# Kernel tuning notes

Hardware: AMD Instinct MI355X
Metric: run time of the kernel (lower is better)

The kernel has to match this reference:

```python
import jax, jax.numpy as jnp
import numpy as np

K = 2  # number of propagation hops (SGConv K)
NEG_SLOPE = 0.1


def setup_inputs() -> dict:
    key = jax.random.key(0)
    k1, k2, k3, k4 = jax.random.split(key, 4)
    N, E, C_in, C_out = 50000, 800000, 128, 512
    x = jax.random.normal(k1, (N, C_in), dtype=jnp.float32)
    edge_index = jax.random.randint(k2, (2, E), 0, N, dtype=jnp.int64)
    W = jax.random.normal(k3, (C_out, C_in), dtype=jnp.float32) * (1.0 / np.sqrt(C_in))
    b = jax.random.normal(k4, (C_out,), dtype=jnp.float32) * 0.01
    return {"x": x, "edge_index": edge_index, "W": W, "b": b}


def reference(x, edge_index, W, b):
    N = x.shape[0]
    # gcn_norm with self-loops (PyG SGConv default: add_self_loops=True)
    loop = jnp.arange(N, dtype=edge_index.dtype)
    src = jnp.concatenate([edge_index[0], loop])  # message sources j
    dst = jnp.concatenate([edge_index[1], loop])  # aggregation targets i
    deg = jax.ops.segment_sum(jnp.ones_like(dst, dtype=x.dtype), dst, num_segments=N)
    dinv = jnp.where(deg > 0, jax.lax.rsqrt(deg), 0.0)
    norm = dinv[src] * dinv[dst]  # [E+N]
    h = x
    for _ in range(K):
        h = jax.ops.segment_sum(norm[:, None] * h[src], dst, num_segments=N)
    y = h @ W.T + b
    return jnp.where(y >= 0, y, NEG_SLOPE * y)  # LeakyReLU(0.1)
```

## Files before the change

kernel.cpp:

```cpp
#include <hip/hip_runtime.h>
#include <hip/hip_bf16.h>

#define CIN 128
#define COUT 512
#define NEG_SLOPE 0.1f

typedef __bf16 bf16x8 __attribute__((ext_vector_type(8)));
typedef float f32x4 __attribute__((ext_vector_type(4)));

static __device__ __forceinline__ unsigned short f2bf(float f) {
  unsigned int u = __builtin_bit_cast(unsigned int, f);
  unsigned int lsb = (u >> 16) & 1u;
  u += 0x7fffu + lsb;
  return (unsigned short)(u >> 16);
}
static __device__ __forceinline__ float bf_lo(unsigned int u) {
  return __builtin_bit_cast(float, u << 16);
}
static __device__ __forceinline__ float bf_hi(unsigned int u) {
  return __builtin_bit_cast(float, u & 0xffff0000u);
}
static __device__ __forceinline__ unsigned int pack2(float lo, float hi) {
  return (unsigned int)f2bf(lo) | ((unsigned int)f2bf(hi) << 16);
}

__global__ void detect_kernel(const int* __restrict__ raw, int* __restrict__ flag, int E) {
  __shared__ int any_nonzero;
  int tid = threadIdx.x;
  if (tid == 0) any_nonzero = 0;
  __syncthreads();
  int v1 = raw[2 * tid + 1];
  int v2 = raw[2 * (E / 2) + 2 * tid + 1];
  if (v1 != 0 || v2 != 0) atomicOr(&any_nonzero, 1);
  __syncthreads();
  if (tid == 0) *flag = any_nonzero ? 0 : 1;
}

__global__ void decode_count_kernel(const int* __restrict__ raw, const int* __restrict__ flag,
                                    int* __restrict__ srcA, int* __restrict__ dstA,
                                    int* __restrict__ cnt, int E, int N) {
  int e = blockIdx.x * blockDim.x + threadIdx.x;
  if (e >= E) return;
  int is64 = *flag;
  int s, d;
  if (is64) {
    s = raw[2 * e];
    d = raw[2 * (E + e)];
  } else {
    s = raw[e];
    d = raw[E + e];
  }
  if ((unsigned)s >= (unsigned)N) s = 0;
  if ((unsigned)d >= (unsigned)N) d = 0;
  srcA[e] = s;
  dstA[e] = d;
  atomicAdd(&cnt[d], 1);
}

__global__ void dinv_kernel(const int* __restrict__ cnt, float* __restrict__ dinv, int N) {
  int i = blockIdx.x * blockDim.x + threadIdx.x;
  if (i < N) dinv[i] = 1.0f / sqrtf((float)(cnt[i] + 1));
}

__global__ __launch_bounds__(256) void xscale_kernel(const float* __restrict__ x,
                                                     const float* __restrict__ dinv,
                                                     unsigned short* __restrict__ xs, int N) {
  int idx = blockIdx.x * blockDim.x + threadIdx.x;
  if (idx >= N * (CIN / 4)) return;
  int row = idx >> 5;
  float d = dinv[row];
  float4 v = ((const float4*)x)[idx];
  ushort4 o;
  o.x = f2bf(v.x * d); o.y = f2bf(v.y * d); o.z = f2bf(v.z * d); o.w = f2bf(v.w * d);
  ((ushort4*)xs)[idx] = o;
}

__global__ __launch_bounds__(256) void scan1_kernel(const int* __restrict__ cnt,
                                                    int* __restrict__ rowptr,
                                                    int* __restrict__ bsum, int N) {
  __shared__ int buf[256];
  int tid = threadIdx.x;
  int base = blockIdx.x * 1024 + tid * 4;
  int v[4];
  int tot = 0;
#pragma unroll
  for (int k = 0; k < 4; ++k) {
    int i = base + k;
    v[k] = (i < N) ? cnt[i] : 0;
    tot += v[k];
  }
  buf[tid] = tot;
  __syncthreads();
  for (int off = 1; off < 256; off <<= 1) {
    int t = (tid >= off) ? buf[tid - off] : 0;
    __syncthreads();
    buf[tid] += t;
    __syncthreads();
  }
  int run = buf[tid] - tot;
  if (tid == 255) bsum[blockIdx.x] = buf[255];
#pragma unroll
  for (int k = 0; k < 4; ++k) {
    int i = base + k;
    if (i < N) rowptr[i] = run;
    run += v[k];
  }
}

__global__ void scan2_kernel(int* __restrict__ bsum, int nb) {
  __shared__ int buf[256];
  int tid = threadIdx.x;
  int v = (tid < nb) ? bsum[tid] : 0;
  buf[tid] = v;
  __syncthreads();
  for (int off = 1; off < 256; off <<= 1) {
    int t = (tid >= off) ? buf[tid - off] : 0;
    __syncthreads();
    buf[tid] += t;
    __syncthreads();
  }
  if (tid < nb) bsum[tid] = buf[tid] - v;
}

__global__ __launch_bounds__(256) void scan3_kernel(int* __restrict__ rowptr,
                                                    const int* __restrict__ bsum,
                                                    int* __restrict__ cursor, int N) {
  int base = blockIdx.x * 1024 + threadIdx.x * 4;
  int off = bsum[blockIdx.x];
#pragma unroll
  for (int k = 0; k < 4; ++k) {
    int i = base + k;
    if (i < N) {
      int r = rowptr[i] + off;
      rowptr[i] = r;
      cursor[i] = r;
    }
  }
}

__global__ void scatter_kernel(const int* __restrict__ srcA, const int* __restrict__ dstA,
                               int* __restrict__ cursor, int* __restrict__ col, int E) {
  int e = blockIdx.x * blockDim.x + threadIdx.x;
  if (e < E) {
    int pos = atomicAdd(&cursor[dstA[e]], 1);
    col[pos] = srcA[e];
  }
}

template <bool SQ>
__global__ __launch_bounds__(256) void hop_kernel(
    const unsigned short* __restrict__ Xs, const float* __restrict__ dinv,
    const int* __restrict__ rowptr, const int* __restrict__ cnt,
    const int* __restrict__ col, unsigned short* __restrict__ Y, int N) {
  int sub = threadIdx.x & 15;
  int node = blockIdx.x * 16 + (threadIdx.x >> 4);
  if (node >= N) return;
  int beg = rowptr[node];
  int num = cnt[node];
  const uint4* X4 = (const uint4*)Xs;
  uint4 self = X4[(size_t)node * 16 + sub];
  float acc[8];
  acc[0] = bf_lo(self.x); acc[1] = bf_hi(self.x);
  acc[2] = bf_lo(self.y); acc[3] = bf_hi(self.y);
  acc[4] = bf_lo(self.z); acc[5] = bf_hi(self.z);
  acc[6] = bf_lo(self.w); acc[7] = bf_hi(self.w);
  int k = 0;
  for (; k + 4 <= num; k += 4) {
    int j0 = col[beg + k];
    int j1 = col[beg + k + 1];
    int j2 = col[beg + k + 2];
    int j3 = col[beg + k + 3];
    uint4 v0 = X4[(size_t)j0 * 16 + sub];
    uint4 v1 = X4[(size_t)j1 * 16 + sub];
    uint4 v2 = X4[(size_t)j2 * 16 + sub];
    uint4 v3 = X4[(size_t)j3 * 16 + sub];
    acc[0] += bf_lo(v0.x); acc[1] += bf_hi(v0.x);
    acc[2] += bf_lo(v0.y); acc[3] += bf_hi(v0.y);
    acc[4] += bf_lo(v0.z); acc[5] += bf_hi(v0.z);
    acc[6] += bf_lo(v0.w); acc[7] += bf_hi(v0.w);
    acc[0] += bf_lo(v1.x); acc[1] += bf_hi(v1.x);
    acc[2] += bf_lo(v1.y); acc[3] += bf_hi(v1.y);
    acc[4] += bf_lo(v1.z); acc[5] += bf_hi(v1.z);
    acc[6] += bf_lo(v1.w); acc[7] += bf_hi(v1.w);
    acc[0] += bf_lo(v2.x); acc[1] += bf_hi(v2.x);
    acc[2] += bf_lo(v2.y); acc[3] += bf_hi(v2.y);
    acc[4] += bf_lo(v2.z); acc[5] += bf_hi(v2.z);
    acc[6] += bf_lo(v2.w); acc[7] += bf_hi(v2.w);
    acc[0] += bf_lo(v3.x); acc[1] += bf_hi(v3.x);
    acc[2] += bf_lo(v3.y); acc[3] += bf_hi(v3.y);
    acc[4] += bf_lo(v3.z); acc[5] += bf_hi(v3.z);
    acc[6] += bf_lo(v3.w); acc[7] += bf_hi(v3.w);
  }
  for (; k < num; ++k) {
    int j0 = col[beg + k];
    uint4 v0 = X4[(size_t)j0 * 16 + sub];
    acc[0] += bf_lo(v0.x); acc[1] += bf_hi(v0.x);
    acc[2] += bf_lo(v0.y); acc[3] += bf_hi(v0.y);
    acc[4] += bf_lo(v0.z); acc[5] += bf_hi(v0.z);
    acc[6] += bf_lo(v0.w); acc[7] += bf_hi(v0.w);
  }
  float di = dinv[node];
  float sc = SQ ? di * di : di;
  uint4 o;
  o.x = pack2(acc[0] * sc, acc[1] * sc);
  o.y = pack2(acc[2] * sc, acc[3] * sc);
  o.z = pack2(acc[4] * sc, acc[5] * sc);
  o.w = pack2(acc[6] * sc, acc[7] * sc);
  ((uint4*)Y)[(size_t)node * 16 + sub] = o;
}

__global__ void wconv_kernel(const float* __restrict__ W, unsigned short* __restrict__ Wbf, int n) {
  int i = blockIdx.x * blockDim.x + threadIdx.x;
  if (i < n) Wbf[i] = f2bf(W[i]);
}

__global__ __launch_bounds__(256) void gemm_kernel(
    const unsigned short* __restrict__ Abf, const unsigned short* __restrict__ Wbf,
    const float* __restrict__ bias, float* __restrict__ out, int M) {
  int wave = threadIdx.x >> 6;
  int lane = threadIdx.x & 63;
  int quad = lane >> 4;
  int l16 = lane & 15;
  int mbase = blockIdx.x * 32;

  bool valid1 = (mbase + 16) < M;

  bf16x8 af[2][4];
#pragma unroll
  for (int kk = 0; kk < 4; ++kk) {
    af[0][kk] = *(const bf16x8*)(Abf + (size_t)(mbase + l16) * CIN + kk * 32 + quad * 8);
    af[1][kk] = valid1
        ? *(const bf16x8*)(Abf + (size_t)(mbase + 16 + l16) * CIN + kk * 32 + quad * 8)
        : bf16x8{};
  }

  int nbase = wave * 128;
#pragma unroll
  for (int nt = 0; nt < 8; ++nt) {
    int n = nbase + nt * 16 + l16;
    const bf16x8* Wrow = (const bf16x8*)(Wbf + (size_t)n * CIN);
    f32x4 acc0 = {}, acc1 = {};
#pragma unroll
    for (int kk = 0; kk < 4; ++kk) {
      bf16x8 bfrag = Wrow[kk * 4 + quad];
      acc0 = __builtin_amdgcn_mfma_f32_16x16x32_bf16(af[0][kk], bfrag, acc0, 0, 0, 0);
      acc1 = __builtin_amdgcn_mfma_f32_16x16x32_bf16(af[1][kk], bfrag, acc1, 0, 0, 0);
    }
    float bv = bias[n];
#pragma unroll
    for (int r = 0; r < 4; ++r) {
      int row0 = mbase + quad * 4 + r;
      float y0 = acc0[r] + bv;
      y0 = (y0 >= 0.f) ? y0 : NEG_SLOPE * y0;
      out[(size_t)row0 * COUT + n] = y0;
      if (valid1) {
        float y1 = acc1[r] + bv;
        y1 = (y1 >= 0.f) ? y1 : NEG_SLOPE * y1;
        out[(size_t)(row0 + 16) * COUT + n] = y1;
      }
    }
  }
}

static inline size_t align_up(size_t v, size_t a) { return (v + a - 1) & ~(a - 1); }

extern "C" void kernel_launch(void* const* d_in, const int* in_sizes, int n_in,
                              void* d_out, int out_size, void* d_ws, size_t ws_size,
                              hipStream_t stream) {
  const float* x = (const float*)d_in[0];
  const int* edge_raw = (const int*)d_in[1];
  const float* W = (const float*)d_in[2];
  const float* b = (const float*)d_in[3];
  float* out = (float*)d_out;

  const int N = in_sizes[0] / CIN;
  const int E = in_sizes[1] / 2;
  const int NB = (N + 1023) / 1024;

  char* w = (char*)d_ws;
  int* flag = (int*)w;            w += align_up(sizeof(int), 256);
  int* bsum = (int*)w;            w += align_up(256 * 4, 256);
  int* cnt = (int*)w;             w += align_up((size_t)N * 4, 256);
  int* rowptr = (int*)w;          w += align_up((size_t)N * 4, 256);
  int* cursor = (int*)w;          w += align_up((size_t)N * 4, 256);
  float* dinv = (float*)w;        w += align_up((size_t)N * 4, 256);
  int* srcA = (int*)w;            w += align_up((size_t)E * 4, 256);
  int* dstA = (int*)w;            w += align_up((size_t)E * 4, 256);
  int* col = (int*)w;             w += align_up((size_t)E * 4, 256);
  unsigned short* h2bf = (unsigned short*)w;  w += align_up((size_t)N * CIN * 2, 256);
  unsigned short* Wbf = (unsigned short*)w;   w += align_up((size_t)COUT * CIN * 2, 256);

  size_t outb = (size_t)out_size * sizeof(float);
  size_t rowb = (size_t)N * CIN * sizeof(unsigned short);
  unsigned short* h1s = (unsigned short*)((char*)d_out + (outb - rowb));
  unsigned short* xs = (unsigned short*)((char*)d_out + (outb - 2 * rowb));

  hipMemsetAsync(cnt, 0, (size_t)N * sizeof(int), stream);

  detect_kernel<<<1, 64, 0, stream>>>(edge_raw, flag, E);
  decode_count_kernel<<<(E + 255) / 256, 256, 0, stream>>>(edge_raw, flag, srcA, dstA, cnt, E, N);
  dinv_kernel<<<(N + 255) / 256, 256, 0, stream>>>(cnt, dinv, N);
  scan1_kernel<<<NB, 256, 0, stream>>>(cnt, rowptr, bsum, N);
  scan2_kernel<<<1, 256, 0, stream>>>(bsum, NB);
  scan3_kernel<<<NB, 256, 0, stream>>>(rowptr, bsum, cursor, N);
  scatter_kernel<<<(E + 255) / 256, 256, 0, stream>>>(srcA, dstA, cursor, col, E);
  xscale_kernel<<<(N * (CIN / 4) + 255) / 256, 256, 0, stream>>>(x, dinv, xs, N);

  hop_kernel<true><<<(N + 15) / 16, 256, 0, stream>>>(xs, dinv, rowptr, cnt, col, h1s, N);
  hop_kernel<false><<<(N + 15) / 16, 256, 0, stream>>>(h1s, dinv, rowptr, cnt, col, h2bf, N);

  wconv_kernel<<<(COUT * CIN + 255) / 256, 256, 0, stream>>>(W, Wbf, COUT * CIN);

  gemm_kernel<<<(N + 31) / 32, 256, 0, stream>>>(h2bf, Wbf, b, out, N);
}
```

Measured before the change: 316.3 us.

## Split hop neighbors across a full wave and reuse atomic rank for CSR scatter

The hop kernel now gives each node a whole 64-lane wave, with four 16-lane groups each gathering a subset of the neighbors and reducing through cross-lane shuffles. This is meant to increase memory-level parallelism for the irregular gathers. The CSR build records each edge's atomic rank during counting, so the scatter needs no second atomic pass and the cursor array goes away. The separate dinv kernel is dropped by recomputing rsqrt inline, the int64 decode uses int2 loads, and the GEMM output stores become nontemporal. The cost is more threads per node, shuffle overhead, and an extra rank array to write and read.

```diff
diff --git a/kernel.cpp b/kernel.cpp
--- a/kernel.cpp
+++ b/kernel.cpp
@@ -38,14 +38,17 @@
 
 __global__ void decode_count_kernel(const int* __restrict__ raw, const int* __restrict__ flag,
                                     int* __restrict__ srcA, int* __restrict__ dstA,
-                                    int* __restrict__ cnt, int E, int N) {
+                                    int* __restrict__ rank, int* __restrict__ cnt,
+                                    int E, int N) {
   int e = blockIdx.x * blockDim.x + threadIdx.x;
   if (e >= E) return;
   int is64 = *flag;
   int s, d;
   if (is64) {
-    s = raw[2 * e];
-    d = raw[2 * (E + e)];
+    int2 sv = ((const int2*)raw)[e];
+    int2 dv = ((const int2*)raw)[E + e];
+    s = sv.x;
+    d = dv.x;
   } else {
     s = raw[e];
     d = raw[E + e];
@@ -54,21 +57,16 @@
   if ((unsigned)d >= (unsigned)N) d = 0;
   srcA[e] = s;
   dstA[e] = d;
-  atomicAdd(&cnt[d], 1);
-}
-
-__global__ void dinv_kernel(const int* __restrict__ cnt, float* __restrict__ dinv, int N) {
-  int i = blockIdx.x * blockDim.x + threadIdx.x;
-  if (i < N) dinv[i] = 1.0f / sqrtf((float)(cnt[i] + 1));
+  rank[e] = atomicAdd(&cnt[d], 1);
 }
 
 __global__ __launch_bounds__(256) void xscale_kernel(const float* __restrict__ x,
-                                                     const float* __restrict__ dinv,
+                                                     const int* __restrict__ cnt,
                                                      unsigned short* __restrict__ xs, int N) {
   int idx = blockIdx.x * blockDim.x + threadIdx.x;
   if (idx >= N * (CIN / 4)) return;
   int row = idx >> 5;
-  float d = dinv[row];
+  float d = 1.0f / sqrtf((float)(cnt[row] + 1));
   float4 v = ((const float4*)x)[idx];
   ushort4 o;
   o.x = f2bf(v.x * d); o.y = f2bf(v.y * d); o.z = f2bf(v.z * d); o.w = f2bf(v.w * d);
@@ -123,53 +121,52 @@
 }
 
 __global__ __launch_bounds__(256) void scan3_kernel(int* __restrict__ rowptr,
-                                                    const int* __restrict__ bsum,
-                                                    int* __restrict__ cursor, int N) {
+                                                    const int* __restrict__ bsum, int N) {
   int base = blockIdx.x * 1024 + threadIdx.x * 4;
   int off = bsum[blockIdx.x];
 #pragma unroll
   for (int k = 0; k < 4; ++k) {
     int i = base + k;
-    if (i < N) {
-      int r = rowptr[i] + off;
-      rowptr[i] = r;
-      cursor[i] = r;
-    }
+    if (i < N) rowptr[i] += off;
   }
 }
 
 __global__ void scatter_kernel(const int* __restrict__ srcA, const int* __restrict__ dstA,
-                               int* __restrict__ cursor, int* __restrict__ col, int E) {
+                               const int* __restrict__ rank, const int* __restrict__ rowptr,
+                               int* __restrict__ col, int E) {
   int e = blockIdx.x * blockDim.x + threadIdx.x;
-  if (e < E) {
-    int pos = atomicAdd(&cursor[dstA[e]], 1);
-    col[pos] = srcA[e];
-  }
+  if (e < E) col[rowptr[dstA[e]] + rank[e]] = srcA[e];
 }
 
 template <bool SQ>
 __global__ __launch_bounds__(256) void hop_kernel(
-    const unsigned short* __restrict__ Xs, const float* __restrict__ dinv,
+    const unsigned short* __restrict__ Xs,
     const int* __restrict__ rowptr, const int* __restrict__ cnt,
     const int* __restrict__ col, unsigned short* __restrict__ Y, int N) {
-  int sub = threadIdx.x & 15;
-  int node = blockIdx.x * 16 + (threadIdx.x >> 4);
+  int lane = threadIdx.x & 63;
+  int wid = threadIdx.x >> 6;
+  int node = blockIdx.x * 4 + wid;
   if (node >= N) return;
+  int sub = lane & 15;
+  int grp = lane >> 4;
   int beg = rowptr[node];
   int num = cnt[node];
   const uint4* X4 = (const uint4*)Xs;
-  uint4 self = X4[(size_t)node * 16 + sub];
-  float acc[8];
-  acc[0] = bf_lo(self.x); acc[1] = bf_hi(self.x);
-  acc[2] = bf_lo(self.y); acc[3] = bf_hi(self.y);
-  acc[4] = bf_lo(self.z); acc[5] = bf_hi(self.z);
-  acc[6] = bf_lo(self.w); acc[7] = bf_hi(self.w);
-  int k = 0;
-  for (; k + 4 <= num; k += 4) {
-    int j0 = col[beg + k];
-    int j1 = col[beg + k + 1];
-    int j2 = col[beg + k + 2];
-    int j3 = col[beg + k + 3];
+  float acc[8] = {0.f, 0.f, 0.f, 0.f, 0.f, 0.f, 0.f, 0.f};
+  if (grp == 0) {
+    uint4 s = X4[(size_t)node * 16 + sub];
+    acc[0] = bf_lo(s.x); acc[1] = bf_hi(s.x);
+    acc[2] = bf_lo(s.y); acc[3] = bf_hi(s.y);
+    acc[4] = bf_lo(s.z); acc[5] = bf_hi(s.z);
+    acc[6] = bf_lo(s.w); acc[7] = bf_hi(s.w);
+  }
+  const int* cp = col + beg;
+  int kb = 0;
+  for (; kb + 16 <= num; kb += 16) {
+    int j0 = cp[kb + grp];
+    int j1 = cp[kb + 4 + grp];
+    int j2 = cp[kb + 8 + grp];
+    int j3 = cp[kb + 12 + grp];
     uint4 v0 = X4[(size_t)j0 * 16 + sub];
     uint4 v1 = X4[(size_t)j1 * 16 + sub];
     uint4 v2 = X4[(size_t)j2 * 16 + sub];
@@ -191,22 +188,31 @@
     acc[4] += bf_lo(v3.z); acc[5] += bf_hi(v3.z);
     acc[6] += bf_lo(v3.w); acc[7] += bf_hi(v3.w);
   }
-  for (; k < num; ++k) {
-    int j0 = col[beg + k];
-    uint4 v0 = X4[(size_t)j0 * 16 + sub];
-    acc[0] += bf_lo(v0.x); acc[1] += bf_hi(v0.x);
-    acc[2] += bf_lo(v0.y); acc[3] += bf_hi(v0.y);
-    acc[4] += bf_lo(v0.z); acc[5] += bf_hi(v0.z);
-    acc[6] += bf_lo(v0.w); acc[7] += bf_hi(v0.w);
-  }
-  float di = dinv[node];
-  float sc = SQ ? di * di : di;
-  uint4 o;
-  o.x = pack2(acc[0] * sc, acc[1] * sc);
-  o.y = pack2(acc[2] * sc, acc[3] * sc);
-  o.z = pack2(acc[4] * sc, acc[5] * sc);
-  o.w = pack2(acc[6] * sc, acc[7] * sc);
-  ((uint4*)Y)[(size_t)node * 16 + sub] = o;
+  for (; kb < num; kb += 4) {
+    int k = kb + grp;
+    if (k < num) {
+      int j0 = cp[k];
+      uint4 v0 = X4[(size_t)j0 * 16 + sub];
+      acc[0] += bf_lo(v0.x); acc[1] += bf_hi(v0.x);
+      acc[2] += bf_lo(v0.y); acc[3] += bf_hi(v0.y);
+      acc[4] += bf_lo(v0.z); acc[5] += bf_hi(v0.z);
+      acc[6] += bf_lo(v0.w); acc[7] += bf_hi(v0.w);
+    }
+  }
+#pragma unroll
+  for (int r = 0; r < 8; ++r) acc[r] += __shfl_xor(acc[r], 16, 64);
+#pragma unroll
+  for (int r = 0; r < 8; ++r) acc[r] += __shfl_xor(acc[r], 32, 64);
+  if (grp == 0) {
+    float di = 1.0f / sqrtf((float)(num + 1));
+    float sc = SQ ? di * di : di;
+    uint4 o;
+    o.x = pack2(acc[0] * sc, acc[1] * sc);
+    o.y = pack2(acc[2] * sc, acc[3] * sc);
+    o.z = pack2(acc[4] * sc, acc[5] * sc);
+    o.w = pack2(acc[6] * sc, acc[7] * sc);
+    ((uint4*)Y)[(size_t)node * 16 + sub] = o;
+  }
 }
 
 __global__ void wconv_kernel(const float* __restrict__ W, unsigned short* __restrict__ Wbf, int n) {
@@ -252,11 +258,11 @@
       int row0 = mbase + quad * 4 + r;
       float y0 = acc0[r] + bv;
       y0 = (y0 >= 0.f) ? y0 : NEG_SLOPE * y0;
-      out[(size_t)row0 * COUT + n] = y0;
+      __builtin_nontemporal_store(y0, &out[(size_t)row0 * COUT + n]);
       if (valid1) {
         float y1 = acc1[r] + bv;
         y1 = (y1 >= 0.f) ? y1 : NEG_SLOPE * y1;
-        out[(size_t)(row0 + 16) * COUT + n] = y1;
+        __builtin_nontemporal_store(y1, &out[(size_t)(row0 + 16) * COUT + n]);
       }
     }
   }
@@ -282,10 +288,9 @@
   int* bsum = (int*)w;            w += align_up(256 * 4, 256);
   int* cnt = (int*)w;             w += align_up((size_t)N * 4, 256);
   int* rowptr = (int*)w;          w += align_up((size_t)N * 4, 256);
-  int* cursor = (int*)w;          w += align_up((size_t)N * 4, 256);
-  float* dinv = (float*)w;        w += align_up((size_t)N * 4, 256);
   int* srcA = (int*)w;            w += align_up((size_t)E * 4, 256);
   int* dstA = (int*)w;            w += align_up((size_t)E * 4, 256);
+  int* rank = (int*)w;            w += align_up((size_t)E * 4, 256);
   int* col = (int*)w;             w += align_up((size_t)E * 4, 256);
   unsigned short* h2bf = (unsigned short*)w;  w += align_up((size_t)N * CIN * 2, 256);
   unsigned short* Wbf = (unsigned short*)w;   w += align_up((size_t)COUT * CIN * 2, 256);
@@ -298,16 +303,15 @@
   hipMemsetAsync(cnt, 0, (size_t)N * sizeof(int), stream);
 
   detect_kernel<<<1, 64, 0, stream>>>(edge_raw, flag, E);
-  decode_count_kernel<<<(E + 255) / 256, 256, 0, stream>>>(edge_raw, flag, srcA, dstA, cnt, E, N);
-  dinv_kernel<<<(N + 255) / 256, 256, 0, stream>>>(cnt, dinv, N);
+  decode_count_kernel<<<(E + 255) / 256, 256, 0, stream>>>(edge_raw, flag, srcA, dstA, rank, cnt, E, N);
   scan1_kernel<<<NB, 256, 0, stream>>>(cnt, rowptr, bsum, N);
   scan2_kernel<<<1, 256, 0, stream>>>(bsum, NB);
-  scan3_kernel<<<NB, 256, 0, stream>>>(rowptr, bsum, cursor, N);
-  scatter_kernel<<<(E + 255) / 256, 256, 0, stream>>>(srcA, dstA, cursor, col, E);
-  xscale_kernel<<<(N * (CIN / 4) + 255) / 256, 256, 0, stream>>>(x, dinv, xs, N);
-
-  hop_kernel<true><<<(N + 15) / 16, 256, 0, stream>>>(xs, dinv, rowptr, cnt, col, h1s, N);
-  hop_kernel<false><<<(N + 15) / 16, 256, 0, stream>>>(h1s, dinv, rowptr, cnt, col, h2bf, N);
+  scan3_kernel<<<NB, 256, 0, stream>>>(rowptr, bsum, N);
+  scatter_kernel<<<(E + 255) / 256, 256, 0, stream>>>(srcA, dstA, rank, rowptr, col, E);
+  xscale_kernel<<<(N * (CIN / 4) + 255) / 256, 256, 0, stream>>>(x, cnt, xs, N);
+
+  hop_kernel<true><<<(N + 3) / 4, 256, 0, stream>>>(xs, rowptr, cnt, col, h1s, N);
+  hop_kernel<false><<<(N + 3) / 4, 256, 0, stream>>>(h1s, rowptr, cnt, col, h2bf, N);
 
   wconv_kernel<<<(COUT * CIN + 255) / 256, 256, 0, stream>>>(W, Wbf, COUT * CIN);
 
```

After: 281.8 us. 10.9% less time.
